# Kernel optimization log

Hardware: AMD Instinct MI355X
Metric: run time of the kernel (lower is better)

## Reference

```python
import jax, jax.numpy as jnp
import numpy as np

B, S, D_IN, D_OUT = 4, 2048, 1024, 1024

def setup_inputs() -> dict:
    key = jax.random.key(0)
    kx, kq, kk, kv = jax.random.split(key, 4)
    x = jax.random.normal(kx, (B, S, D_IN), dtype=jnp.float32)
    # torch nn.Linear weight is [d_out, d_in]; we store the transposed [d_in, d_out]
    # so y = x @ W, scaled like default init to keep magnitudes sane.
    scale = 1.0 / np.sqrt(D_IN)
    Wq = jax.random.normal(kq, (D_IN, D_OUT), dtype=jnp.float32) * scale
    Wk = jax.random.normal(kk, (D_IN, D_OUT), dtype=jnp.float32) * scale
    Wv = jax.random.normal(kv, (D_IN, D_OUT), dtype=jnp.float32) * scale
    return {"x": x, "Wq": Wq, "Wk": Wk, "Wv": Wv}

def reference(x, Wq, Wk, Wv):
    b, n, _ = x.shape
    q = jnp.einsum('bnd,de->bne', x, Wq)   # [B,S,D_OUT]
    k = jnp.einsum('bnd,de->bne', x, Wk)
    v = jnp.einsum('bnd,de->bne', x, Wv)
    scores = jnp.einsum('bqe,bke->bqk', q, k) / jnp.sqrt(jnp.float32(k.shape[-1]))
    causal = jnp.triu(jnp.ones((n, n), dtype=bool), k=1)  # True above diagonal -> masked
    scores = jnp.where(causal[None, :, :], -jnp.inf, scores)
    weights = jax.nn.softmax(scores, axis=-1)
    # dropout p=0.0 (deterministic baseline) -> identity
    context = jnp.einsum('bqk,bke->bqe', weights, v)
    return context
```

## Files before the change

kernel.cpp:

```cpp
#include <hip/hip_runtime.h>
#include <hip/hip_bf16.h>

#define BB 4
#define SS 2048
#define DD 1024

typedef __attribute__((ext_vector_type(8))) short bf16x8;
typedef __attribute__((ext_vector_type(4))) float f32x4;

__device__ __forceinline__ ushort f2bf(float f) {
  unsigned u = __float_as_uint(f);
  unsigned r = (u + 0x7fffu + ((u >> 16) & 1u)) >> 16;
  return (ushort)r;
}

__device__ __forceinline__ void gload_lds16(const void* g, void* l) {
  __builtin_amdgcn_global_load_lds(
      (const __attribute__((address_space(1))) void*)g,
      (__attribute__((address_space(3))) void*)l, 16, 0, 0);
}

__global__ __launch_bounds__(256) void cast_x_kernel(const float* __restrict__ x,
                                                     ushort* __restrict__ xb) {
  const int i = blockIdx.x * 256 + threadIdx.x;
  const float4 a = ((const float4*)x)[2 * i];
  const float4 b = ((const float4*)x)[2 * i + 1];
  ushort4 o0, o1;
  o0.x = f2bf(a.x); o0.y = f2bf(a.y); o0.z = f2bf(a.z); o0.w = f2bf(a.w);
  o1.x = f2bf(b.x); o1.y = f2bf(b.y); o1.z = f2bf(b.z); o1.w = f2bf(b.w);
  ((ushort4*)xb)[2 * i] = o0;
  ((ushort4*)xb)[2 * i + 1] = o1;
}

__global__ __launch_bounds__(256) void cast_transpose_w(const float* __restrict__ W0,
                                                        const float* __restrict__ W1,
                                                        const float* __restrict__ W2,
                                                        ushort* __restrict__ Wt) {
  const float* W = blockIdx.z == 0 ? W0 : (blockIdx.z == 1 ? W1 : W2);
  ushort* O = Wt + (size_t)blockIdx.z * DD * DD;
  __shared__ ushort t[32][33];
  const int n0 = blockIdx.x * 32, k0 = blockIdx.y * 32;
  const int tx = threadIdx.x, ty = threadIdx.y;
#pragma unroll
  for (int j = 0; j < 4; j++) {
    int k = k0 + ty + j * 8;
    t[ty + j * 8][tx] = f2bf(W[(size_t)k * DD + n0 + tx]);
  }
  __syncthreads();
#pragma unroll
  for (int j = 0; j < 4; j++) {
    int n = ty + j * 8;
    O[(size_t)(n0 + n) * DD + k0 + tx] = t[tx][n];
  }
}

__global__ __launch_bounds__(256) void transpose_v(const ushort* __restrict__ V, int ldv,
                                                   ushort* __restrict__ Vt) {
  const int b = blockIdx.z;
  const ushort* Vb = V + (size_t)b * SS * ldv;
  ushort* Ob = Vt + (size_t)b * DD * SS;
  __shared__ ushort t[32][33];
  const int d0 = blockIdx.x * 32, s0 = blockIdx.y * 32;
  const int tx = threadIdx.x, ty = threadIdx.y;
#pragma unroll
  for (int j = 0; j < 4; j++) {
    int s = s0 + ty + j * 8;
    t[ty + j * 8][tx] = Vb[(size_t)s * ldv + d0 + tx];
  }
  __syncthreads();
#pragma unroll
  for (int j = 0; j < 4; j++) {
    int d = ty + j * 8;
    Ob[(size_t)(d0 + d) * SS + s0 + tx] = t[tx][d];
  }
}

template <int BM, int BN, bool TRI, bool EXPMASK, bool KCLIP, bool DIVL, bool OUT_BF16>
__global__ __launch_bounds__(512) void gemm8(const ushort* __restrict__ A, int lda, size_t strA,
                                             const ushort* __restrict__ Bt, int ldb, size_t strB,
                                             void* __restrict__ C, int ldc, size_t strC, int K) {
  constexpr int LA = BM / 64;
  constexpr int LB = BN / 64;
  constexpr int FM = BM / 32;
  constexpr int FN = BN / 64;
  int nb, mb, bz;
  if (TRI) {
    constexpr int NMB = SS / BM;
    constexpr int T = NMB * (NMB + 1) / 2;
    int flat = blockIdx.x + T * blockIdx.z;
    flat = (flat & 7) * ((T * BB) >> 3) + (flat >> 3);
    bz = flat / T;
    int i = flat % T;
    mb = (int)((sqrtf(8.f * i + 1.f) - 1.f) * 0.5f);
    while ((mb + 1) * (mb + 2) / 2 <= i) ++mb;
    while (mb * (mb + 1) / 2 > i) --mb;
    nb = i - mb * (mb + 1) / 2;
  } else {
    nb = blockIdx.x; mb = blockIdx.y; bz = blockIdx.z;
  }
  const ushort* Ab = A + (size_t)bz * strA;
  const ushort* Bb = Bt + (size_t)bz * strB;

  __shared__ ushort lds[2][(BM + BN) * 64];

  const int tid = threadIdx.x;
  const int lane = tid & 63;
  const int wid = tid >> 6;
  const int wr = wid >> 2, wc = wid & 3;
  const int fr = lane & 15, qq = lane >> 4;
  const int sx = (fr & 7) << 4;

  int kEnd = KCLIP ? (mb + 1) * BM : K;
  if (kEnd > K) kEnd = K;
  const int NT = kEnd >> 6;

  auto stage = [&](int kt, int buf) {
    ushort* As = &lds[buf][0];
    ushort* Bs = &lds[buf][BM * 64];
    const ushort* ga = Ab + (size_t)mb * BM * lda + kt * 64;
    const ushort* gb = Bb + (size_t)nb * BN * ldb + kt * 64;
#pragma unroll
    for (int j = 0; j < LA; j++) {
      int D = (j * 512 + tid) * 16;
      int r = D >> 7;
      int cb = (D & 127) ^ ((r & 7) << 4);
      gload_lds16(ga + (size_t)r * lda + (cb >> 1), (char*)As + D);
    }
#pragma unroll
    for (int j = 0; j < LB; j++) {
      int D = (j * 512 + tid) * 16;
      int r = D >> 7;
      int cb = (D & 127) ^ ((r & 7) << 4);
      gload_lds16(gb + (size_t)r * ldb + (cb >> 1), (char*)Bs + D);
    }
  };

  stage(0, 0);
  if (NT > 1) stage(1, 1);

  f32x4 acc[FM][FN] = {};
  float lsum[FM];
#pragma unroll
  for (int i = 0; i < FM; i++) lsum[i] = 0.f;

  for (int kt = 0; kt < NT; ++kt) {
    const int cur = kt & 1;
    if (kt < NT - 1) {
      if constexpr (LA + LB == 6) asm volatile("s_waitcnt vmcnt(6)" ::: "memory");
      else if constexpr (LA + LB == 4) asm volatile("s_waitcnt vmcnt(4)" ::: "memory");
      else asm volatile("s_waitcnt vmcnt(0)" ::: "memory");
    } else {
      asm volatile("s_waitcnt vmcnt(0)" ::: "memory");
    }
    __builtin_amdgcn_s_barrier();
    __builtin_amdgcn_sched_barrier(0);

    const char* As = (const char*)&lds[cur][0];
    const char* Bs = (const char*)&lds[cur][BM * 64];
    __builtin_amdgcn_s_setprio(1);
#pragma unroll
    for (int ks = 0; ks < 2; ++ks) {
      const int kb = ks * 64 + qq * 16;
      bf16x8 a[FM], b[FN];
#pragma unroll
      for (int i = 0; i < FM; i++) {
        int r = wr * (BM / 2) + i * 16 + fr;
        a[i] = *(const bf16x8*)(As + r * 128 + (kb ^ sx));
      }
#pragma unroll
      for (int j = 0; j < FN; j++) {
        int r = wc * (BN / 4) + j * 16 + fr;
        b[j] = *(const bf16x8*)(Bs + r * 128 + (kb ^ sx));
      }
      if (DIVL && wc == 0) {
#pragma unroll
        for (int i = 0; i < FM; i++)
#pragma unroll
          for (int e = 0; e < 8; e++)
            lsum[i] += __uint_as_float((unsigned)(unsigned short)a[i][e] << 16);
      }
#pragma unroll
      for (int i = 0; i < FM; i++)
#pragma unroll
        for (int j = 0; j < FN; j++)
          acc[i][j] = __builtin_amdgcn_mfma_f32_16x16x32_bf16(a[i], b[j], acc[i][j], 0, 0, 0);
    }
    __builtin_amdgcn_s_setprio(0);
    __builtin_amdgcn_s_barrier();
    __builtin_amdgcn_sched_barrier(0);
    if (kt + 2 < NT) stage(kt + 2, cur);
  }

  __shared__ float lds_l[2][BM / 2];
  if (DIVL) {
    if (wc == 0) {
#pragma unroll
      for (int i = 0; i < FM; i++) {
        lsum[i] += __shfl_xor(lsum[i], 16);
        lsum[i] += __shfl_xor(lsum[i], 32);
      }
      if (qq == 0) {
#pragma unroll
        for (int i = 0; i < FM; i++) lds_l[wr][i * 16 + fr] = lsum[i];
      }
    }
    __syncthreads();
  }

  const int col0 = nb * BN + wc * (BN / 4) + fr;
  const int row00 = mb * BM + wr * (BM / 2) + qq * 4;
  if (OUT_BF16) {
    ushort* Cb = (ushort*)C + (size_t)bz * strC;
#pragma unroll
    for (int i = 0; i < FM; i++)
#pragma unroll
      for (int rr = 0; rr < 4; rr++) {
        const int row = row00 + i * 16 + rr;
        size_t ro = (size_t)row * ldc;
#pragma unroll
        for (int j = 0; j < FN; j++) {
          float v = acc[i][j][rr];
          if (EXPMASK) {
            v = __expf(v * 0.03125f);
            if (col0 + j * 16 > row) v = 0.f;
          }
          Cb[ro + col0 + j * 16] = f2bf(v);
        }
      }
  } else {
    float* Cb = (float*)C + (size_t)bz * strC;
#pragma unroll
    for (int i = 0; i < FM; i++)
#pragma unroll
      for (int rr = 0; rr < 4; rr++) {
        size_t ro = (size_t)(row00 + i * 16 + rr) * ldc;
        float invl = 1.f;
        if (DIVL) invl = 1.f / lds_l[wr][i * 16 + qq * 4 + rr];
#pragma unroll
        for (int j = 0; j < FN; j++) Cb[ro + col0 + j * 16] = acc[i][j][rr] * invl;
      }
  }
}

extern "C" void kernel_launch(void* const* d_in, const int* in_sizes, int n_in,
                              void* d_out, int out_size, void* d_ws, size_t ws_size,
                              hipStream_t stream) {
  const float* x = (const float*)d_in[0];
  const float* Wq = (const float*)d_in[1];
  const float* Wk = (const float*)d_in[2];
  const float* Wv = (const float*)d_in[3];

  char* ws = (char*)d_ws;
  ushort* xb = (ushort*)(ws);
  ushort* Wt = (ushort*)(ws + 16777216);
  ushort* QKV = (ushort*)(ws + 23068672);
  ushort* P = (ushort*)(ws + 73400320);
  ushort* Vt = (ushort*)(ws);

  const size_t SD = (size_t)SS * DD;
  const size_t S2 = (size_t)SS * SS;
  const size_t SQ = (size_t)SS * 3072;

  cast_x_kernel<<<(BB * SS * DD) / (256 * 8), 256, 0, stream>>>(x, xb);
  cast_transpose_w<<<dim3(DD / 32, DD / 32, 3), dim3(32, 8), 0, stream>>>(Wq, Wk, Wv, Wt);
  gemm8<128, 128, false, false, false, false, true>
      <<<dim3(3072 / 128, (BB * SS) / 128, 1), 512, 0, stream>>>(
          xb, DD, 0, Wt, DD, 0, QKV, 3072, 0, DD);
  transpose_v<<<dim3(DD / 32, SS / 32, BB), dim3(32, 8), 0, stream>>>(QKV + 2048, 3072, Vt);
  gemm8<128, 128, true, true, false, false, true><<<dim3(136, 1, BB), 512, 0, stream>>>(
      QKV, 3072, SQ, QKV + 1024, 3072, SQ, P, SS, S2, DD);
  gemm8<128, 128, false, false, true, true, false>
      <<<dim3(DD / 128, SS / 128, BB), 512, 0, stream>>>(
          P, SS, S2, Vt, SS, SD, d_out, DD, SD, SS);

  (void)in_sizes; (void)n_in; (void)out_size; (void)ws_size;
}
```

Before: 163.5 us.

## Compute V transposed directly via swapped GEMM, drop transpose kernel, balance PV grid

Splits the fused QKV projection into a QK GEMM and a separate V GEMM that computes Wv^T·x^T, so V comes out already transposed ([D, B*S]) and the standalone transpose_v kernel goes away. The PV GEMM now reads Vt with a B*S leading dimension and per-batch offset of 2048 columns. A new BAL flag reverses row-block order for half the batches in the causal PV GEMM, so that blocks with long and short K ranges are mixed across the grid for better load balance. The cost is an extra kernel launch and a V GEMM whose output layout has a long stride.

Result: faster. 152.7 us (-6.6%).

```diff
diff --git a/kernel.cpp b/kernel.cpp
--- a/kernel.cpp
+++ b/kernel.cpp
@@ -54,28 +54,8 @@
   }
 }
 
-__global__ __launch_bounds__(256) void transpose_v(const ushort* __restrict__ V, int ldv,
-                                                   ushort* __restrict__ Vt) {
-  const int b = blockIdx.z;
-  const ushort* Vb = V + (size_t)b * SS * ldv;
-  ushort* Ob = Vt + (size_t)b * DD * SS;
-  __shared__ ushort t[32][33];
-  const int d0 = blockIdx.x * 32, s0 = blockIdx.y * 32;
-  const int tx = threadIdx.x, ty = threadIdx.y;
-#pragma unroll
-  for (int j = 0; j < 4; j++) {
-    int s = s0 + ty + j * 8;
-    t[ty + j * 8][tx] = Vb[(size_t)s * ldv + d0 + tx];
-  }
-  __syncthreads();
-#pragma unroll
-  for (int j = 0; j < 4; j++) {
-    int d = ty + j * 8;
-    Ob[(size_t)(d0 + d) * SS + s0 + tx] = t[tx][d];
-  }
-}
-
-template <int BM, int BN, bool TRI, bool EXPMASK, bool KCLIP, bool DIVL, bool OUT_BF16>
+template <int BM, int BN, bool TRI, bool EXPMASK, bool KCLIP, bool DIVL, bool BAL,
+          bool OUT_BF16>
 __global__ __launch_bounds__(512) void gemm8(const ushort* __restrict__ A, int lda, size_t strA,
                                              const ushort* __restrict__ Bt, int ldb, size_t strB,
                                              void* __restrict__ C, int ldc, size_t strC, int K) {
@@ -97,6 +77,7 @@
     nb = i - mb * (mb + 1) / 2;
   } else {
     nb = blockIdx.x; mb = blockIdx.y; bz = blockIdx.z;
+    if (BAL && (blockIdx.z & 2)) mb = (gridDim.y - 1) - mb;
   }
   const ushort* Ab = A + (size_t)bz * strA;
   const ushort* Bb = Bt + (size_t)bz * strB;
@@ -253,25 +234,28 @@
   char* ws = (char*)d_ws;
   ushort* xb = (ushort*)(ws);
   ushort* Wt = (ushort*)(ws + 16777216);
-  ushort* QKV = (ushort*)(ws + 23068672);
+  ushort* QK = (ushort*)(ws + 23068672);
+  ushort* Vt = (ushort*)(ws + 56623104);
   ushort* P = (ushort*)(ws + 73400320);
-  ushort* Vt = (ushort*)(ws);
 
   const size_t SD = (size_t)SS * DD;
   const size_t S2 = (size_t)SS * SS;
-  const size_t SQ = (size_t)SS * 3072;
+  const size_t SQ2 = (size_t)SS * 2048;
 
   cast_x_kernel<<<(BB * SS * DD) / (256 * 8), 256, 0, stream>>>(x, xb);
   cast_transpose_w<<<dim3(DD / 32, DD / 32, 3), dim3(32, 8), 0, stream>>>(Wq, Wk, Wv, Wt);
-  gemm8<128, 128, false, false, false, false, true>
-      <<<dim3(3072 / 128, (BB * SS) / 128, 1), 512, 0, stream>>>(
-          xb, DD, 0, Wt, DD, 0, QKV, 3072, 0, DD);
-  transpose_v<<<dim3(DD / 32, SS / 32, BB), dim3(32, 8), 0, stream>>>(QKV + 2048, 3072, Vt);
-  gemm8<128, 128, true, true, false, false, true><<<dim3(136, 1, BB), 512, 0, stream>>>(
-      QKV, 3072, SQ, QKV + 1024, 3072, SQ, P, SS, S2, DD);
-  gemm8<128, 128, false, false, true, true, false>
+  gemm8<128, 128, false, false, false, false, false, true>
+      <<<dim3(2048 / 128, (BB * SS) / 128, 1), 512, 0, stream>>>(
+          xb, DD, 0, Wt, DD, 0, QK, 2048, 0, DD);
+  gemm8<128, 128, false, false, false, false, false, true>
+      <<<dim3((BB * SS) / 128, DD / 128, 1), 512, 0, stream>>>(
+          Wt + 2 * DD * DD, DD, 0, xb, DD, 0, Vt, BB * SS, 0, DD);
+  gemm8<128, 128, true, true, false, false, false, true>
+      <<<dim3(136, 1, BB), 512, 0, stream>>>(
+          QK, 2048, SQ2, QK + 1024, 2048, SQ2, P, SS, S2, DD);
+  gemm8<128, 128, false, false, true, true, true, false>
       <<<dim3(DD / 128, SS / 128, BB), 512, 0, stream>>>(
-          P, SS, S2, Vt, SS, SD, d_out, DD, SD, SS);
+          P, SS, S2, Vt, BB * SS, 2048, d_out, DD, SD, SS);
 
   (void)in_sizes; (void)n_in; (void)out_size; (void)ws_size;
 }
```
